# Kernel tuning notes

Hardware: AMD Instinct MI355X
Metric: run time of the kernel (lower is better)

The kernel has to match this reference:

```python
import jax, jax.numpy as jnp
import numpy as np

HF8_BIAS = 14  # exponent bias for the 1-4-3 hf8 layout; HF8_MAX = 2^(15-14)*1.875 = 3.75


def hf8_decode(bits):
    """Decode 8-bit hf8 codes (1 sign, 4 exp, 3 mantissa) to float.

    Mirrors convert.hf8_to_fp16: an elementwise dequant producing the
    fp16-valued weight tensor (computed here in fp32 for reference accuracy).
    """
    bits = bits.astype(jnp.int32)
    sign = jnp.where(((bits >> 7) & 1) == 1, -1.0, 1.0)
    exp = (bits >> 3) & 0xF
    man = (bits & 0x7).astype(jnp.float32)
    normal = jnp.exp2((exp - HF8_BIAS).astype(jnp.float32)) * (1.0 + man / 8.0)
    subnormal = jnp.exp2(jnp.float32(1 - HF8_BIAS)) * (man / 8.0)
    return sign * jnp.where(exp == 0, subnormal, normal)


def setup_inputs() -> dict:
    key = jax.random.key(0)
    k1, k2, k3 = jax.random.split(key, 3)
    B, Cin, Cout, H, W, K = 8, 320, 320, 64, 64, 3
    x = jax.random.normal(k1, (B, Cin, H, W), dtype=jnp.float32)
    w_bits = jax.random.randint(k2, (Cout, Cin, K, K), 0, 256, dtype=jnp.int32)
    b_bits = jax.random.randint(k3, (Cout,), 0, 256, dtype=jnp.int32)
    return {"x": x, "w_bits": w_bits, "b_bits": b_bits}


def reference(x, w_bits, b_bits):
    # dequant hf8 -> dense weight/bias (the fusible elementwise pass)
    w = hf8_decode(w_bits)          # [Cout, Cin, K, K]
    b = hf8_decode(b_bits)          # [Cout]
    # padding_mode == 'zeros' branch: plain conv2d, stride 1, pad 1, dilation 1, groups 1
    out = jax.lax.conv_general_dilated(
        x, w,
        window_strides=(1, 1),
        padding=((1, 1), (1, 1)),
        rhs_dilation=(1, 1),
        dimension_numbers=("NCHW", "OIHW", "NCHW"),
        feature_group_count=1,
    )
    return out + b[None, :, None, None]
```

## Files before the change

kernel.cpp:

```cpp
#include <hip/hip_runtime.h>
#include <stdint.h>

typedef short v8s __attribute__((ext_vector_type(8)));
typedef float v4f __attribute__((ext_vector_type(4)));
typedef unsigned int u32;

#define CIN   320
#define COUT  320
#define HH    64
#define WW    64
#define BN    80
#define NT    10
#define WLB   15360
#define WKHB  61440

__device__ __forceinline__ float hf8_decode_f(int b) {
    int e = (b >> 3) & 15;
    int m = b & 7;
    float v = ldexpf((float)(e ? (8 + m) : m), e ? (e - 17) : -16);
    return ((b >> 7) & 1) ? -v : v;
}

__device__ __forceinline__ u32 cvt_pk_bf16(float lo, float hi) {
    u32 r;
    asm("v_cvt_pk_bf16_f32 %0, %1, %2" : "=v"(r) : "v"(lo), "v"(hi));
    return r;
}

__device__ __forceinline__ void gload16(const void* g, void* l) {
    __builtin_amdgcn_global_load_lds(
        (const __attribute__((address_space(1))) u32*)(uintptr_t)g,
        (__attribute__((address_space(3))) u32*)(uintptr_t)l, 16, 0, 0);
}

__global__ void dequant_kernel(const int* __restrict__ w_bits,
                               const int* __restrict__ b_bits,
                               unsigned short* __restrict__ w_deq2,
                               float* __restrict__ b_deq) {
    int o  = blockIdx.x * 256 + threadIdx.x;
    int e  = o & 7;
    int c2 = o >> 3;
    int co = c2 % COUT;
    int c3 = c2 / COUT;
    int cig = c3 & 3;
    int c4 = c3 >> 2;
    int kw = c4 % 3;
    int c5 = c4 / 3;
    int kh = c5 % 3;
    int t  = c5 / 3;
    int ci = t * 32 + cig * 8 + e;
    float v = hf8_decode_f(w_bits[(co * CIN + ci) * 9 + kh * 3 + kw] & 0xFF);
    w_deq2[o] = (unsigned short)(__float_as_uint(v) >> 16);
    if (o < COUT) b_deq[o] = hf8_decode_f(b_bits[o] & 0xFF);
}

__global__ __launch_bounds__(256, 2) void conv_phase_kernel(
        const float* __restrict__ x,
        const unsigned short* __restrict__ w_deq2,
        const float* __restrict__ b_deq,
        float* __restrict__ out) {
    __shared__ __align__(16) unsigned short xs[6 * 66 * 32];
    __shared__ __align__(16) unsigned short wl[2 * WLB / 2];

    const int tid  = threadIdx.x;
    const int bid  = blockIdx.x;
    const int cob  = bid >> 7;
    const int mb   = bid & 127;
    const int n    = mb >> 4;
    const int h0   = (mb & 15) << 2;
    const int wave = tid >> 6;
    const int lane = tid & 63;
    const int lhi  = lane >> 4;
    const int llo  = lane & 15;
    const int ciL2 = tid & 15;
    const int seg  = tid >> 4;

    if (tid < 192) {
        int row = tid >> 5, rem = tid & 31;
        int side = rem >> 4, e = rem & 15;
        *(u32*)((char*)xs + row * 4224 + side * 4160 + e * 4) = 0;
    }

    int woffW[4];
    #pragma unroll
    for (int ii = 0; ii < 4; ++ii) {
        int i = wave * 4 + ii;
        int c = i * 64 + lane;
        int q = c / BN;
        int co = c - q * BN;
        woffW[ii] = (q * COUT + cob * BN + co) << 4;
    }

    v4f acc[4][5];
    #pragma unroll
    for (int i = 0; i < 4; ++i)
        #pragma unroll
        for (int j = 0; j < 5; ++j)
            acc[i][j] = (v4f){0.f, 0.f, 0.f, 0.f};

    float4 xa[6], xbv[6];
    const float* xpl = x + ((size_t)(n * CIN) + 2 * ciL2) * (HH * WW);

    auto issueW = [&](int t_, int kh_, int wb) {
        const char* base = (const char*)w_deq2 + (size_t)(t_ * 3 + kh_) * WKHB;
        char* dst = (char*)wl + wb * WLB + wave * 4096;
        #pragma unroll
        for (int ii = 0; ii < 4; ++ii) {
            if (wave * 4 + ii < 15)
                gload16(base + woffW[ii], dst + ii * 1024);
        }
    };
    auto loadX = [&](int tt) {
        const float* xp0 = xpl + (size_t)(tt * 32) * (HH * WW);
        const float* xp1 = xp0 + HH * WW;
        #pragma unroll
        for (int r = 0; r < 6; ++r) {
            int gh = h0 - 1 + r;
            if (gh >= 0 && gh < HH) {
                xa[r]  = *(const float4*)(xp0 + gh * WW + seg * 4);
                xbv[r] = *(const float4*)(xp1 + gh * WW + seg * 4);
            } else {
                xa[r]  = make_float4(0.f, 0.f, 0.f, 0.f);
                xbv[r] = make_float4(0.f, 0.f, 0.f, 0.f);
            }
        }
    };
    auto cvtWriteX = [&]() {
        #pragma unroll
        for (int r = 0; r < 6; ++r) {
            u32 p0 = cvt_pk_bf16(xa[r].x, xbv[r].x);
            u32 p1 = cvt_pk_bf16(xa[r].y, xbv[r].y);
            u32 p2 = cvt_pk_bf16(xa[r].z, xbv[r].z);
            u32 p3 = cvt_pk_bf16(xa[r].w, xbv[r].w);
            char* c0 = (char*)xs + r * 4224 + (1 + seg * 4) * 64 + ciL2 * 4;
            *(u32*)(c0)       = p0;
            *(u32*)(c0 + 64)  = p1;
            *(u32*)(c0 + 128) = p2;
            *(u32*)(c0 + 192) = p3;
        }
    };
    auto computeKh = [&](int kh, int wb) {
        const char* xp = (const char*)xs + (wave + kh) * 4224;
        const unsigned short* wp = wl + wb * (WLB / 2);
        __builtin_amdgcn_s_setprio(1);
        #pragma unroll
        for (int kw = 0; kw < 3; ++kw) {
            v8s bfr[5];
            #pragma unroll
            for (int nr = 0; nr < 5; ++nr)
                bfr[nr] = *(const v8s*)&wp[((kw * 4 + lhi) * BN + nr * 16 + llo) * 8];
            #pragma unroll
            for (int mr = 0; mr < 4; ++mr) {
                v8s afr = *(const v8s*)(xp + (mr * 16 + llo + kw) * 64 + lhi * 16);
                #pragma unroll
                for (int nr = 0; nr < 5; ++nr)
                    acc[mr][nr] = __builtin_amdgcn_mfma_f32_16x16x32_bf16(
                        afr, bfr[nr], acc[mr][nr], 0, 0, 0);
            }
        }
        __builtin_amdgcn_s_setprio(0);
    };

    issueW(0, 0, 0);
    loadX(0);
    cvtWriteX();

    for (int t = 0; t < NT; ++t) {
        const int p = t & 1;
        __syncthreads();
        issueW(t, 1, p ^ 1);
        computeKh(0, p);
        __syncthreads();
        issueW(t, 2, p);
        if (t + 1 < NT) loadX(t + 1);
        computeKh(1, p ^ 1);
        __syncthreads();
        if (t + 1 < NT) issueW(t + 1, 0, p ^ 1);
        computeKh(2, p);
        __syncthreads();
        if (t + 1 < NT) cvtWriteX();
    }

    const int h = h0 + wave;
    #pragma unroll
    for (int nr = 0; nr < 5; ++nr) {
        int co = cob * BN + nr * 16 + llo;
        float bias = b_deq[co];
        float* op = out + ((size_t)(n * COUT + co) * HH + h) * WW;
        #pragma unroll
        for (int mr = 0; mr < 4; ++mr) {
            int wc = mr * 16 + lhi * 4;
            float4 o;
            o.x = acc[mr][nr][0] + bias;
            o.y = acc[mr][nr][1] + bias;
            o.z = acc[mr][nr][2] + bias;
            o.w = acc[mr][nr][3] + bias;
            *(float4*)(op + wc) = o;
        }
    }
}

extern "C" void kernel_launch(void* const* d_in, const int* in_sizes, int n_in,
                              void* d_out, int out_size, void* d_ws, size_t ws_size,
                              hipStream_t stream) {
    const float* x      = (const float*)d_in[0];
    const int*   w_bits = (const int*)d_in[1];
    const int*   b_bits = (const int*)d_in[2];
    float*       out    = (float*)d_out;

    unsigned short* w_deq2 = (unsigned short*)d_ws;
    float*          b_deq  = (float*)((char*)d_ws + 1843200);

    dequant_kernel<<<3600, 256, 0, stream>>>(w_bits, b_bits, w_deq2, b_deq);
    conv_phase_kernel<<<512, 256, 0, stream>>>(x, w_deq2, b_deq, out);
}
```

Before: 70.87 us.

## Pre-transpose x to bf16 in a prepass and load it into LDS asynchronously

The dequant kernel now also converts x into a padded, channel-interleaved bf16 layout in workspace (fused into one launch). The conv kernel then streams x tiles straight into double-buffered LDS with global_load_lds instead of loading fp32 into registers and converting. It also halves the block to 128 threads, with each wave computing two output rows. This removes the in-loop conversion and its register staging and one barrier per iteration. In exchange it adds an extra global round-trip of x in bf16 and reduces waves per CU.

```diff
diff --git a/kernel.cpp b/kernel.cpp
--- a/kernel.cpp
+++ b/kernel.cpp
@@ -11,6 +11,7 @@
 #define WW    64
 #define BN    80
 #define NT    10
+#define XSB   25344
 #define WLB   15360
 #define WKHB  61440
 
@@ -33,33 +34,75 @@
         (__attribute__((address_space(3))) u32*)(uintptr_t)l, 16, 0, 0);
 }
 
-__global__ void dequant_kernel(const int* __restrict__ w_bits,
-                               const int* __restrict__ b_bits,
-                               unsigned short* __restrict__ w_deq2,
-                               float* __restrict__ b_deq) {
-    int o  = blockIdx.x * 256 + threadIdx.x;
-    int e  = o & 7;
-    int c2 = o >> 3;
-    int co = c2 % COUT;
-    int c3 = c2 / COUT;
-    int cig = c3 & 3;
-    int c4 = c3 >> 2;
-    int kw = c4 % 3;
-    int c5 = c4 / 3;
-    int kh = c5 % 3;
-    int t  = c5 / 3;
-    int ci = t * 32 + cig * 8 + e;
-    float v = hf8_decode_f(w_bits[(co * CIN + ci) * 9 + kh * 3 + kw] & 0xFF);
-    w_deq2[o] = (unsigned short)(__float_as_uint(v) >> 16);
-    if (o < COUT) b_deq[o] = hf8_decode_f(b_bits[o] & 0xFF);
-}
-
-__global__ __launch_bounds__(256, 2) void conv_phase_kernel(
-        const float* __restrict__ x,
+__global__ __launch_bounds__(256) void prepass_kernel(const int* __restrict__ w_bits,
+                                                      const int* __restrict__ b_bits,
+                                                      const float* __restrict__ x,
+                                                      unsigned short* __restrict__ w_deq2,
+                                                      float* __restrict__ b_deq,
+                                                      unsigned short* __restrict__ x_t) {
+    __shared__ __align__(16) unsigned short lt[32 * 64];
+    const int tid = threadIdx.x;
+    if (blockIdx.x < 3600) {
+        int o  = blockIdx.x * 256 + tid;
+        int e  = o & 7;
+        int c2 = o >> 3;
+        int co = c2 % COUT;
+        int c3 = c2 / COUT;
+        int cig = c3 & 3;
+        int c4 = c3 >> 2;
+        int kw = c4 % 3;
+        int c5 = c4 / 3;
+        int kh = c5 % 3;
+        int t  = c5 / 3;
+        int ci = t * 32 + cig * 8 + e;
+        float v = hf8_decode_f(w_bits[(co * CIN + ci) * 9 + kh * 3 + kw] & 0xFF);
+        w_deq2[o] = (unsigned short)(__float_as_uint(v) >> 16);
+        if (o < COUT) b_deq[o] = hf8_decode_f(b_bits[o] & 0xFF);
+        return;
+    }
+    const int b  = blockIdx.x - 3600;
+    const int hp = b % 66;
+    const int nc = b / 66;
+    char* outp = (char*)x_t + (size_t)b * 4096;
+    if (hp == 0 || hp == 65) {
+        *(int4*)(outp + tid * 16) = make_int4(0, 0, 0, 0);
+        return;
+    }
+    const int h = hp - 1;
+    {
+        int ci = tid >> 3, wg = tid & 7;
+        const float* src = x + ((size_t)nc * 32 + ci) * (HH * WW) + h * WW + wg * 8;
+        float4 a = *(const float4*)src;
+        float4 c = *(const float4*)(src + 4);
+        u32 d0 = cvt_pk_bf16(a.x, a.y);
+        u32 d1 = cvt_pk_bf16(a.z, a.w);
+        u32 d2 = cvt_pk_bf16(c.x, c.y);
+        u32 d3 = cvt_pk_bf16(c.z, c.w);
+        *(int4*)&lt[ci * 64 + wg * 8] = make_int4(d0, d1, d2, d3);
+    }
+    __syncthreads();
+    if (tid < 128) {
+        int w2 = tid & 31, o = tid >> 5;
+        u32 A[4], B[4];
+        #pragma unroll
+        for (int j = 0; j < 4; ++j) {
+            int p = o * 4 + j;
+            u32 de = *(const u32*)&lt[(2 * p) * 64 + w2 * 2];
+            u32 dq = *(const u32*)&lt[(2 * p + 1) * 64 + w2 * 2];
+            A[j] = __builtin_amdgcn_perm(dq, de, 0x05040100u);
+            B[j] = __builtin_amdgcn_perm(dq, de, 0x07060302u);
+        }
+        *(int4*)(outp + (2 * w2) * 64 + o * 16)     = make_int4(A[0], A[1], A[2], A[3]);
+        *(int4*)(outp + (2 * w2 + 1) * 64 + o * 16) = make_int4(B[0], B[1], B[2], B[3]);
+    }
+}
+
+__global__ __launch_bounds__(128, 1) void conv_phase_kernel(
+        const unsigned short* __restrict__ x_t,
         const unsigned short* __restrict__ w_deq2,
         const float* __restrict__ b_deq,
         float* __restrict__ out) {
-    __shared__ __align__(16) unsigned short xs[6 * 66 * 32];
+    __shared__ __align__(16) unsigned short xs[2 * XSB / 2];
     __shared__ __align__(16) unsigned short wl[2 * WLB / 2];
 
     const int tid  = threadIdx.x;
@@ -72,75 +115,57 @@
     const int lane = tid & 63;
     const int lhi  = lane >> 4;
     const int llo  = lane & 15;
-    const int ciL2 = tid & 15;
-    const int seg  = tid >> 4;
-
-    if (tid < 192) {
-        int row = tid >> 5, rem = tid & 31;
+
+    for (int i = tid; i < 384; i += 128) {
+        int buf = i / 192;
+        int r   = (i - buf * 192) >> 5;
+        int rem = i & 31;
         int side = rem >> 4, e = rem & 15;
-        *(u32*)((char*)xs + row * 4224 + side * 4160 + e * 4) = 0;
-    }
-
-    int woffW[4];
+        *(u32*)((char*)xs + buf * XSB + r * 4224 + side * 4160 + e * 4) = 0;
+    }
+
+    int woffW[8];
     #pragma unroll
-    for (int ii = 0; ii < 4; ++ii) {
-        int i = wave * 4 + ii;
-        int c = i * 64 + lane;
+    for (int k = 0; k < 8; ++k) {
+        int c = k * 128 + tid;
         int q = c / BN;
         int co = c - q * BN;
-        woffW[ii] = (q * COUT + cob * BN + co) << 4;
-    }
-
-    v4f acc[4][5];
+        woffW[k] = (q * COUT + cob * BN + co) << 4;
+    }
+
+    v4f acc[2][4][5];
     #pragma unroll
-    for (int i = 0; i < 4; ++i)
-        #pragma unroll
-        for (int j = 0; j < 5; ++j)
-            acc[i][j] = (v4f){0.f, 0.f, 0.f, 0.f};
-
-    float4 xa[6], xbv[6];
-    const float* xpl = x + ((size_t)(n * CIN) + 2 * ciL2) * (HH * WW);
+    for (int r = 0; r < 2; ++r)
+        #pragma unroll
+        for (int wc = 0; wc < 4; ++wc)
+            #pragma unroll
+            for (int j = 0; j < 5; ++j)
+                acc[r][wc][j] = (v4f){0.f, 0.f, 0.f, 0.f};
+
+    const char* xt_base = (const char*)x_t + ((size_t)(n * NT) * 66 + h0) * 4096;
 
     auto issueW = [&](int t_, int kh_, int wb) {
         const char* base = (const char*)w_deq2 + (size_t)(t_ * 3 + kh_) * WKHB;
-        char* dst = (char*)wl + wb * WLB + wave * 4096;
-        #pragma unroll
-        for (int ii = 0; ii < 4; ++ii) {
-            if (wave * 4 + ii < 15)
-                gload16(base + woffW[ii], dst + ii * 1024);
+        char* dst = (char*)wl + wb * WLB + tid * 16;
+        #pragma unroll
+        for (int k = 0; k < 8; ++k) {
+            if (k * 128 + tid < 960)
+                gload16(base + woffW[k], dst + k * 2048);
         }
     };
-    auto loadX = [&](int tt) {
-        const float* xp0 = xpl + (size_t)(tt * 32) * (HH * WW);
-        const float* xp1 = xp0 + HH * WW;
-        #pragma unroll
-        for (int r = 0; r < 6; ++r) {
-            int gh = h0 - 1 + r;
-            if (gh >= 0 && gh < HH) {
-                xa[r]  = *(const float4*)(xp0 + gh * WW + seg * 4);
-                xbv[r] = *(const float4*)(xp1 + gh * WW + seg * 4);
-            } else {
-                xa[r]  = make_float4(0.f, 0.f, 0.f, 0.f);
-                xbv[r] = make_float4(0.f, 0.f, 0.f, 0.f);
-            }
+    auto issueX = [&](int t_, int xb) {
+        const char* src = xt_base + (size_t)t_ * (66 * 4096);
+        char* dstb = (char*)xs + xb * XSB;
+        #pragma unroll
+        for (int k = 0; k < 12; ++k) {
+            int c = k * 128 + tid;
+            int j = c >> 8;
+            int u = c & 255;
+            gload16(src + j * 4096 + u * 16, dstb + j * 4224 + 64 + u * 16);
         }
     };
-    auto cvtWriteX = [&]() {
-        #pragma unroll
-        for (int r = 0; r < 6; ++r) {
-            u32 p0 = cvt_pk_bf16(xa[r].x, xbv[r].x);
-            u32 p1 = cvt_pk_bf16(xa[r].y, xbv[r].y);
-            u32 p2 = cvt_pk_bf16(xa[r].z, xbv[r].z);
-            u32 p3 = cvt_pk_bf16(xa[r].w, xbv[r].w);
-            char* c0 = (char*)xs + r * 4224 + (1 + seg * 4) * 64 + ciL2 * 4;
-            *(u32*)(c0)       = p0;
-            *(u32*)(c0 + 64)  = p1;
-            *(u32*)(c0 + 128) = p2;
-            *(u32*)(c0 + 192) = p3;
-        }
-    };
-    auto computeKh = [&](int kh, int wb) {
-        const char* xp = (const char*)xs + (wave + kh) * 4224;
+    auto computeKh = [&](int kh, int xb, int wb) {
+        const char* xp = (const char*)xs + xb * XSB + (2 * wave + kh) * 4224;
         const unsigned short* wp = wl + wb * (WLB / 2);
         __builtin_amdgcn_s_setprio(1);
         #pragma unroll
@@ -150,52 +175,52 @@
             for (int nr = 0; nr < 5; ++nr)
                 bfr[nr] = *(const v8s*)&wp[((kw * 4 + lhi) * BN + nr * 16 + llo) * 8];
             #pragma unroll
-            for (int mr = 0; mr < 4; ++mr) {
-                v8s afr = *(const v8s*)(xp + (mr * 16 + llo + kw) * 64 + lhi * 16);
+            for (int r = 0; r < 2; ++r)
                 #pragma unroll
-                for (int nr = 0; nr < 5; ++nr)
-                    acc[mr][nr] = __builtin_amdgcn_mfma_f32_16x16x32_bf16(
-                        afr, bfr[nr], acc[mr][nr], 0, 0, 0);
-            }
+                for (int wc = 0; wc < 4; ++wc) {
+                    v8s afr = *(const v8s*)(xp + r * 4224 + (wc * 16 + llo + kw) * 64 + lhi * 16);
+                    #pragma unroll
+                    for (int nr = 0; nr < 5; ++nr)
+                        acc[r][wc][nr] = __builtin_amdgcn_mfma_f32_16x16x32_bf16(
+                            afr, bfr[nr], acc[r][wc][nr], 0, 0, 0);
+                }
         }
         __builtin_amdgcn_s_setprio(0);
     };
 
     issueW(0, 0, 0);
-    loadX(0);
-    cvtWriteX();
+    issueX(0, 0);
 
     for (int t = 0; t < NT; ++t) {
         const int p = t & 1;
         __syncthreads();
         issueW(t, 1, p ^ 1);
-        computeKh(0, p);
+        computeKh(0, p, p);
         __syncthreads();
         issueW(t, 2, p);
-        if (t + 1 < NT) loadX(t + 1);
-        computeKh(1, p ^ 1);
+        computeKh(1, p, p ^ 1);
         __syncthreads();
-        if (t + 1 < NT) issueW(t + 1, 0, p ^ 1);
-        computeKh(2, p);
-        __syncthreads();
-        if (t + 1 < NT) cvtWriteX();
-    }
-
-    const int h = h0 + wave;
+        if (t + 1 < NT) { issueW(t + 1, 0, p ^ 1); issueX(t + 1, p ^ 1); }
+        computeKh(2, p, p);
+    }
+
     #pragma unroll
     for (int nr = 0; nr < 5; ++nr) {
         int co = cob * BN + nr * 16 + llo;
         float bias = b_deq[co];
-        float* op = out + ((size_t)(n * COUT + co) * HH + h) * WW;
-        #pragma unroll
-        for (int mr = 0; mr < 4; ++mr) {
-            int wc = mr * 16 + lhi * 4;
-            float4 o;
-            o.x = acc[mr][nr][0] + bias;
-            o.y = acc[mr][nr][1] + bias;
-            o.z = acc[mr][nr][2] + bias;
-            o.w = acc[mr][nr][3] + bias;
-            *(float4*)(op + wc) = o;
+        #pragma unroll
+        for (int r = 0; r < 2; ++r) {
+            int h = h0 + 2 * wave + r;
+            float* op = out + ((size_t)(n * COUT + co) * HH + h) * WW + lhi * 4;
+            #pragma unroll
+            for (int wc = 0; wc < 4; ++wc) {
+                float4 o;
+                o.x = acc[r][wc][nr][0] + bias;
+                o.y = acc[r][wc][nr][1] + bias;
+                o.z = acc[r][wc][nr][2] + bias;
+                o.w = acc[r][wc][nr][3] + bias;
+                *(float4*)(op + wc * 16) = o;
+            }
         }
     }
 }
@@ -210,7 +235,8 @@
 
     unsigned short* w_deq2 = (unsigned short*)d_ws;
     float*          b_deq  = (float*)((char*)d_ws + 1843200);
-
-    dequant_kernel<<<3600, 256, 0, stream>>>(w_bits, b_bits, w_deq2, b_deq);
-    conv_phase_kernel<<<512, 256, 0, stream>>>(x, w_deq2, b_deq, out);
-}
+    unsigned short* x_t    = (unsigned short*)((char*)d_ws + (2u << 20));
+
+    prepass_kernel<<<8880, 256, 0, stream>>>(w_bits, b_bits, x, w_deq2, b_deq, x_t);
+    conv_phase_kernel<<<512, 128, 0, stream>>>(x_t, w_deq2, b_deq, out);
+}
```

Result: slower. 74.19 us (+4.7%).
